# Kernel tuning notes

Measured on AMD Instinct MI355X. Metric: run time of the kernel, lower is better.

Reference implementation:

```python
import jax, jax.numpy as jnp
import numpy as np
from jax import lax
from jax.scipy.linalg import solve_triangular

T, DX, DZ = 8192, 1024, 16
POS_CONST = 1e-6
THRESH = 1e-5


def setup_inputs() -> dict:
    key = jax.random.key(0)
    ks = jax.random.split(key, 7)
    s = 0.02  # small init scale so A ~ I and AA is well-conditioned for Cholesky
    return {
        "X": jax.random.normal(ks[0], (T, DX), jnp.float32),
        "W1": jax.random.normal(ks[1], (DX, DX), jnp.float32) * s,
        "b1": jnp.zeros((DX,), jnp.float32),
        "Wmu": jax.random.normal(ks[2], (DX, DZ), jnp.float32) * s,
        "bmu": jnp.zeros((DZ,), jnp.float32),
        "WA": jax.random.normal(ks[3], (DX, DZ * DZ), jnp.float32) * s,
        "bA": jnp.zeros((DZ * DZ,), jnp.float32),
        "WB": jax.random.normal(ks[4], (2 * DX, DZ * DZ), jnp.float32) * s,
        "bB": jnp.zeros((DZ * DZ,), jnp.float32),
        "eps": jax.random.normal(ks[5], (T, DZ), jnp.float32),
    }


def _blk_tridag_chol(AA, BB):
    # AA: (T, d, d) diagonal blocks, BB: (T-1, d, d) lower off-diagonal blocks.
    # Returns lower-bidiagonal block Cholesky: chol_A (T,d,d), chol_B (T-1,d,d).
    L0 = jnp.linalg.cholesky(AA[0])

    def step(Lprev, ins):
        Bt, At = ins
        # C = Bt @ inv(Lprev)^T, via triangular solve: Lprev C^T = Bt^T
        C = solve_triangular(Lprev, Bt.T, lower=True).T
        Lt = jnp.linalg.cholesky(At - C @ C.T)
        return Lt, (Lt, C)

    _, (Ls, Cs) = lax.scan(step, L0, (BB, AA[1:]))
    return jnp.concatenate([L0[None], Ls]), Cs


def _blk_chol_inv_identity(chol_A, chol_B):
    # Forward substitution L x = b with b = block-diagonal identity blocks.
    I = jnp.eye(DZ, dtype=chol_A.dtype)
    x0 = solve_triangular(chol_A[0], I, lower=True)

    def step(xprev, ins):
        Lt, Ct = ins
        xt = solve_triangular(Lt, I - Ct @ xprev, lower=True)
        return xt, xt

    _, xs = lax.scan(step, x0, (chol_A[1:], chol_B))
    return jnp.concatenate([x0[None], xs])


def reference(X, W1, b1, Wmu, bmu, WA, bA, WB, bB, eps):
    # encode
    h = jax.nn.relu(X @ W1 + b1)                       # (T, dx)
    mu = h @ Wmu + bmu                                 # (T, dz)
    A = (h @ WA + bA).reshape(T, DZ, DZ) + jnp.eye(DZ, dtype=X.dtype)
    hcat = jnp.concatenate([h[1:], h[:-1]], axis=1)    # (T-1, 2*dx)
    B = (hcat @ WB + bB).reshape(T - 1, DZ, DZ)

    # make_psd
    diag_sq = jnp.einsum('tij,tkj->tik', A, A)         # A A^T
    offd_sq = jnp.einsum('tij,tkj->tik', B, B)         # B B^T
    offd_sq = jnp.concatenate([jnp.zeros((1, DZ, DZ), X.dtype), offd_sq])
    AA = diag_sq + offd_sq + POS_CONST * jnp.eye(DZ, dtype=X.dtype)
    BB = jnp.einsum('tij,tkj->tik', B, A[:-1])         # B A[:-1]^T

    chol_A, chol_B = _blk_tridag_chol(AA, BB)
    r = _blk_chol_inv_identity(chol_A, chol_B)         # (T, dz, dz)

    # relu(r - thresh) + thresh == max(r, thresh)
    r = jax.nn.relu(r - THRESH) + THRESH
    logdet = -jnp.log(jnp.einsum('tii->ti', r)).sum()
    entropy = logdet + DX * T / 2.0 * (1.0 + np.log(2.0 * np.pi))

    # sample_z = mu + r^T eps per block
    sample_z = mu + jnp.einsum('tji,tj->ti', r, eps)
    return entropy, sample_z
```

## Files before the change

### kernel.cpp

```cpp
#include <hip/hip_runtime.h>
#include <math.h>


#define T_STEPS 8192
#define DXX 1024

typedef __bf16 bf16x8 __attribute__((ext_vector_type(8)));
typedef float f32x4 __attribute__((ext_vector_type(4)));
typedef unsigned short u16x8 __attribute__((ext_vector_type(8)));
typedef unsigned short u16x4 __attribute__((ext_vector_type(4)));

#define DOT4(r, b) ((r).x*(b).x + (r).y*(b).y + (r).z*(b).z + (r).w*(b).w)

__device__ __forceinline__ unsigned short f2bf(float v) {
  unsigned int u = __float_as_uint(v);
  unsigned int r = (u + 0x7FFFu + ((u >> 16) & 1u)) >> 16;
  return (unsigned short)r;
}
__device__ __forceinline__ float bf2f(unsigned short b) {
  return __uint_as_float(((unsigned int)b) << 16);
}

__global__ __launch_bounds__(256) void to_bf16(
    const float* __restrict__ src, unsigned short* __restrict__ dst, int n4)
{
  int idx = blockIdx.x * 256 + threadIdx.x;
  if (idx >= n4) return;
  float4 v = ((const float4*)src)[idx];
  u16x4 h;
  h[0] = f2bf(v.x); h[1] = f2bf(v.y); h[2] = f2bf(v.z); h[3] = f2bf(v.w);
  *(u16x4*)(dst + (size_t)idx * 4) = h;
}

__global__ __launch_bounds__(256) void transpose_bf16(
    const float* __restrict__ W, unsigned short* __restrict__ Tt, int K, int N)
{
  __shared__ float tile[32][33];
  int k0 = blockIdx.x * 32, n0 = blockIdx.y * 32;
  int c = threadIdx.x & 31, r = threadIdx.x >> 5;
#pragma unroll
  for (int e = 0; e < 4; ++e)
    tile[r + 8 * e][c] = W[(size_t)(k0 + r + 8 * e) * N + n0 + c];
  __syncthreads();
#pragma unroll
  for (int e = 0; e < 4; ++e)
    Tt[(size_t)(n0 + r + 8 * e) * K + k0 + c] = f2bf(tile[c][r + 8 * e]);
}

#define LDT 40

__global__ __launch_bounds__(256) void gemm_mfma(
    const unsigned short* __restrict__ Abf, const unsigned short* __restrict__ Bbf,
    const float* __restrict__ bias, int biasN, float* __restrict__ outF,
    unsigned short* __restrict__ outBf, int M, int N, int K, int mode)
{
  __shared__ __align__(16) unsigned short At[128 * LDT];
  __shared__ __align__(16) unsigned short Bt[128 * LDT];
  int tid = threadIdx.x;
  int l = tid & 63;
  int w = tid >> 6;
  int wm = w >> 1, wn = w & 1;
  int lane15 = l & 15, quad = l >> 4;
  int bm = blockIdx.y * 128, bn = blockIdx.x * 128;
  int srow = tid >> 1, shalf = tid & 1;
  const size_t aRowOff = (size_t)(bm + srow) * K;
  const size_t bRowOff = (size_t)(bn + srow) * K;

  f32x4 acc[4][4];
#pragma unroll
  for (int mi = 0; mi < 4; ++mi)
#pragma unroll
    for (int ni = 0; ni < 4; ++ni) acc[mi][ni] = (f32x4){0.f, 0.f, 0.f, 0.f};

  for (int k0 = 0; k0 < K; k0 += 32) {
    u16x8 a0 = *(const u16x8*)(Abf + aRowOff + k0 + shalf * 16);
    u16x8 a1 = *(const u16x8*)(Abf + aRowOff + k0 + shalf * 16 + 8);
    u16x8 b0 = *(const u16x8*)(Bbf + bRowOff + k0 + shalf * 16);
    u16x8 b1 = *(const u16x8*)(Bbf + bRowOff + k0 + shalf * 16 + 8);
    __syncthreads();
    *(u16x8*)&At[srow * LDT + shalf * 16] = a0;
    *(u16x8*)&At[srow * LDT + shalf * 16 + 8] = a1;
    *(u16x8*)&Bt[srow * LDT + shalf * 16] = b0;
    *(u16x8*)&Bt[srow * LDT + shalf * 16 + 8] = b1;
    __syncthreads();
    bf16x8 af[4], bfr[4];
#pragma unroll
    for (int mi = 0; mi < 4; ++mi)
      af[mi] = *(const bf16x8*)&At[(wm * 64 + mi * 16 + lane15) * LDT + quad * 8];
#pragma unroll
    for (int ni = 0; ni < 4; ++ni)
      bfr[ni] = *(const bf16x8*)&Bt[(wn * 64 + ni * 16 + lane15) * LDT + quad * 8];
#pragma unroll
    for (int mi = 0; mi < 4; ++mi)
#pragma unroll
      for (int ni = 0; ni < 4; ++ni)
        acc[mi][ni] = __builtin_amdgcn_mfma_f32_16x16x32_bf16(af[mi], bfr[ni], acc[mi][ni], 0, 0, 0);
  }

#pragma unroll
  for (int mi = 0; mi < 4; ++mi) {
#pragma unroll
    for (int ni = 0; ni < 4; ++ni) {
      int gc = bn + wn * 64 + ni * 16 + lane15;
      float bv = (bias && gc < biasN) ? bias[gc] : 0.f;
#pragma unroll
      for (int r = 0; r < 4; ++r) {
        int gr = bm + wm * 64 + mi * 16 + quad * 4 + r;
        float v = acc[mi][ni][r] + bv;
        if (mode == 1) {
          outBf[(size_t)gr * N + gc] = f2bf(fmaxf(v, 0.f));
        } else {
          outF[(size_t)gr * N + gc] = v;
        }
      }
    }
  }
}

__global__ __launch_bounds__(256) void mu_gemm(
    const unsigned short* __restrict__ hbf, const float* __restrict__ Wmu,
    const float* __restrict__ bmu, float* __restrict__ mu)
{
  int idx = blockIdx.x * 256 + threadIdx.x;
  int t = idx >> 4, j = idx & 15;
  const u16x8* ph = (const u16x8*)(hbf + (size_t)t * 1024);
  float s = bmu[j];
#pragma unroll 2
  for (int k8 = 0; k8 < 128; ++k8) {
    u16x8 hv = ph[k8];
#pragma unroll
    for (int e = 0; e < 8; ++e)
      s = fmaf(bf2f(hv[e]), Wmu[(k8 * 8 + e) * 16 + j], s);
  }
  mu[idx] = s;
}

__global__ __launch_bounds__(256) void make_psd(
    const float* __restrict__ Ccat, const float* __restrict__ bB,
    float* __restrict__ AA, float* __restrict__ BBm, float* __restrict__ logdet)
{
  int t = blockIdx.x;
  int tid = threadIdx.x;
  int i = tid >> 4, j = tid & 15;
  if (t == 0 && tid == 0) *logdet = 0.f;
  __shared__ float a[16][17], bp[16][17], bq[16][17];
  a[i][j] = Ccat[(size_t)t * 768 + tid] + (i == j ? 1.f : 0.f);
  bp[i][j] = (t >= 1) ? (Ccat[(size_t)t * 768 + 256 + tid] + Ccat[(size_t)(t - 1) * 768 + 512 + tid] + bB[tid]) : 0.f;
  bool has_b = (t < T_STEPS - 1);
  if (has_b) bq[i][j] = Ccat[(size_t)(t + 1) * 768 + 256 + tid] + Ccat[(size_t)t * 768 + 512 + tid] + bB[tid];
  __syncthreads();
  float s = (i == j) ? 1e-6f : 0.f;
#pragma unroll
  for (int k = 0; k < 16; ++k) s += a[i][k] * a[j][k] + bp[i][k] * bp[j][k];
  AA[(size_t)t * 256 + tid] = s;
  if (has_b) {
    float s2 = 0.f;
#pragma unroll
    for (int k = 0; k < 16; ++k) s2 += bq[i][k] * a[j][k];
    BBm[(size_t)t * 256 + tid] = s2;
  }
}

#define RIC_S 4
#define RIC_W 16
#define RIC_NCH (T_STEPS / RIC_S)

__global__ __launch_bounds__(64) void riccati_wave(
    const float* __restrict__ AA, const float* __restrict__ BBm,
    float* __restrict__ D)
{
  int l = threadIdx.x;
  int q = l >> 4, c = l & 15;
  int p = blockIdx.x;
  int t0 = p * RIC_S;
  int tw = t0 - RIC_W; if (tw < 0) tw = 0;
  int tend = t0 + RIC_S - 1;
  int row = l >> 2, cb = (l & 3) * 4;

  __shared__ float bbs[320], dis[320], ys[320];

  float dr[4];
#pragma unroll
  for (int u = 0; u < 4; ++u)
    dr[u] = AA[(size_t)tw * 256 + (q * 4 + u) * 16 + c];

  for (int t = tw; ; ++t) {
    if (t >= t0) {
#pragma unroll
      for (int u = 0; u < 4; ++u)
        D[(size_t)t * 256 + (q * 4 + u) * 16 + c] = dr[u];
    }
    if (t == tend) break;
    float4 bb4 = *(const float4*)(BBm + (size_t)t * 256 + l * 4);
    float aar[4];
#pragma unroll
    for (int u = 0; u < 4; ++u)
      aar[u] = AA[(size_t)(t + 1) * 256 + (q * 4 + u) * 16 + c];

#pragma unroll
    for (int k = 0; k < 16; ++k) {
      const int kq = k >> 2, ku = k & 3;
      float rowv = __shfl(dr[ku], (kq << 4) | c);
      float pv   = __shfl(dr[ku], (kq << 4) | k);
      float cv0  = __shfl(dr[0], (l & 48) | k);
      float cv1  = __shfl(dr[1], (l & 48) | k);
      float cv2  = __shfl(dr[2], (l & 48) | k);
      float cv3  = __shfl(dr[3], (l & 48) | k);
      float rpv  = __builtin_amdgcn_rcpf(pv);
      float t1v  = rowv * rpv;
      float cva[4] = {cv0, cv1, cv2, cv3};
#pragma unroll
      for (int u = 0; u < 4; ++u) {
        bool irow = (q == kq) && (u == ku);
        float nv = irow ? ((c == k) ? rpv : t1v)
                        : ((c == k) ? (-cva[u] * rpv) : fmaf(-cva[u], t1v, dr[u]));
        dr[u] = nv;
      }
    }

    *(float4*)&bbs[row * 20 + cb] = bb4;
#pragma unroll
    for (int u = 0; u < 4; ++u) dis[(q * 4 + u) * 20 + c] = dr[u];

    float y0a = 0, y1a = 0, y2a = 0, y3a = 0;
    float y0b = 0, y1b = 0, y2b = 0, y3b = 0;
#pragma unroll
    for (int kb = 0; kb < 4; ++kb) {
      float4 bc4 = *(const float4*)&bbs[c * 20 + kb * 4];
      float4 r0 = *(const float4*)&dis[(q * 4 + 0) * 20 + kb * 4];
      float4 r1 = *(const float4*)&dis[(q * 4 + 1) * 20 + kb * 4];
      float4 r2 = *(const float4*)&dis[(q * 4 + 2) * 20 + kb * 4];
      float4 r3 = *(const float4*)&dis[(q * 4 + 3) * 20 + kb * 4];
      if (kb & 1) {
        y0b += DOT4(r0, bc4); y1b += DOT4(r1, bc4); y2b += DOT4(r2, bc4); y3b += DOT4(r3, bc4);
      } else {
        y0a += DOT4(r0, bc4); y1a += DOT4(r1, bc4); y2a += DOT4(r2, bc4); y3a += DOT4(r3, bc4);
      }
    }
    ys[(q * 4 + 0) * 20 + c] = y0a + y0b;
    ys[(q * 4 + 1) * 20 + c] = y1a + y1b;
    ys[(q * 4 + 2) * 20 + c] = y2a + y2b;
    ys[(q * 4 + 3) * 20 + c] = y3a + y3b;

    float s0a = aar[0], s1a = aar[1], s2a = aar[2], s3a = aar[3];
    float s0b = 0, s1b = 0, s2b = 0, s3b = 0;
#pragma unroll
    for (int kb = 0; kb < 4; ++kb) {
      float4 b0 = *(const float4*)&bbs[(q * 4 + 0) * 20 + kb * 4];
      float4 b1 = *(const float4*)&bbs[(q * 4 + 1) * 20 + kb * 4];
      float4 b2 = *(const float4*)&bbs[(q * 4 + 2) * 20 + kb * 4];
      float4 b3 = *(const float4*)&bbs[(q * 4 + 3) * 20 + kb * 4];
      float yk0 = ys[(kb * 4 + 0) * 20 + c];
      float yk1 = ys[(kb * 4 + 1) * 20 + c];
      float yk2 = ys[(kb * 4 + 2) * 20 + c];
      float yk3 = ys[(kb * 4 + 3) * 20 + c];
      if (kb & 1) {
        s0b -= b0.x * yk0 + b0.y * yk1 + b0.z * yk2 + b0.w * yk3;
        s1b -= b1.x * yk0 + b1.y * yk1 + b1.z * yk2 + b1.w * yk3;
        s2b -= b2.x * yk0 + b2.y * yk1 + b2.z * yk2 + b2.w * yk3;
        s3b -= b3.x * yk0 + b3.y * yk1 + b3.z * yk2 + b3.w * yk3;
      } else {
        s0a -= b0.x * yk0 + b0.y * yk1 + b0.z * yk2 + b0.w * yk3;
        s1a -= b1.x * yk0 + b1.y * yk1 + b1.z * yk2 + b1.w * yk3;
        s2a -= b2.x * yk0 + b2.y * yk1 + b2.z * yk2 + b2.w * yk3;
        s3a -= b3.x * yk0 + b3.y * yk1 + b3.z * yk2 + b3.w * yk3;
      }
    }
    dr[0] = s0a + s0b; dr[1] = s1a + s1b; dr[2] = s2a + s2b; dr[3] = s3a + s3b;
  }
}

__global__ __launch_bounds__(256) void chol_inv(
    const float* __restrict__ D, const float* __restrict__ BBm,
    float* __restrict__ Linv, float* __restrict__ Cmat)
{
  int t = blockIdx.x;
  int tid = threadIdx.x;
  int i = tid >> 4, j = tid & 15;
  __shared__ float d[16][17], li[16][17], rhs[16][17], bb[16][17];
  d[i][j] = D[(size_t)t * 256 + tid];
  bool has_b = (t < T_STEPS - 1);
  if (has_b) bb[i][j] = BBm[(size_t)t * 256 + tid];
  rhs[i][j] = (i == j) ? 1.f : 0.f;
  __syncthreads();
  for (int k = 0; k < 16; ++k) {
    if (tid == k * 16 + k) d[k][k] = sqrtf(d[k][k]);
    __syncthreads();
    if (j == k && i > k) d[i][k] /= d[k][k];
    __syncthreads();
    if (i > k && j > k && j <= i) d[i][j] -= d[i][k] * d[j][k];
    __syncthreads();
  }
  for (int k = 0; k < 16; ++k) {
    if (i == k) li[k][j] = rhs[k][j] / d[k][k];
    __syncthreads();
    if (i > k) rhs[i][j] -= d[i][k] * li[k][j];
    __syncthreads();
  }
  Linv[(size_t)t * 256 + tid] = li[i][j];
  if (has_b) {
    float s = 0.f;
#pragma unroll
    for (int k = 0; k < 16; ++k) s += bb[i][k] * li[j][k];
    Cmat[(size_t)t * 256 + tid] = s;
  }
}

__global__ __launch_bounds__(256) void gmat_kernel(
    const float* __restrict__ Linv, const float* __restrict__ Cmat,
    float* __restrict__ Gmat)
{
  int t = blockIdx.x;
  int tid = threadIdx.x;
  int i = tid >> 4, j = tid & 15;
  if (t == 0) { Gmat[tid] = 0.f; return; }
  __shared__ float li[16][17], cm[16][17];
  li[i][j] = Linv[(size_t)t * 256 + tid];
  cm[i][j] = Cmat[(size_t)(t - 1) * 256 + tid];
  __syncthreads();
  float s = 0.f;
#pragma unroll
  for (int k = 0; k < 16; ++k) s -= li[i][k] * cm[k][j];
  Gmat[(size_t)t * 256 + tid] = s;
}

#define XS 8
#define XW 32
#define XNCH (T_STEPS / XS)

__global__ __launch_bounds__(64) void xseq_g(
    const float* __restrict__ Linv, const float* __restrict__ Gmat,
    const float* __restrict__ mu, const float* __restrict__ eps,
    float* __restrict__ out, float* __restrict__ logdet)
{
  int l = threadIdx.x;
  int q = l >> 4, c = l & 15;
  int p = blockIdx.x;
  int t0 = p * XS;
  int ts = t0 - XW; if (ts < 0) ts = 0;
  int row = l >> 2, cb = (l & 3) * 4;
  __shared__ float gs[320];
  float xr[4] = {0.f, 0.f, 0.f, 0.f};
  float logacc = 0.f;

  float4 g4 = *(const float4*)(Gmat + (size_t)ts * 256 + l * 4);
  float li[4];
#pragma unroll
  for (int u = 0; u < 4; ++u)
    li[u] = Linv[(size_t)ts * 256 + (q * 4 + u) * 16 + c];

  for (int t = ts; t < t0 + XS; ++t) {
    float4 g4n = {0.f, 0.f, 0.f, 0.f};
    float lin[4] = {0.f, 0.f, 0.f, 0.f};
    if (t + 1 < t0 + XS) {
      g4n = *(const float4*)(Gmat + (size_t)(t + 1) * 256 + l * 4);
#pragma unroll
      for (int u = 0; u < 4; ++u)
        lin[u] = Linv[(size_t)(t + 1) * 256 + (q * 4 + u) * 16 + c];
    }
    *(float4*)&gs[row * 20 + cb] = g4;

    float x0a = li[0], x1a = li[1], x2a = li[2], x3a = li[3];
    float x0b = 0.f, x1b = 0.f, x2b = 0.f, x3b = 0.f;
#pragma unroll
    for (int kb = 0; kb < 4; ++kb) {
      float4 r0 = *(const float4*)&gs[(q * 4 + 0) * 20 + kb * 4];
      float4 r1 = *(const float4*)&gs[(q * 4 + 1) * 20 + kb * 4];
      float4 r2 = *(const float4*)&gs[(q * 4 + 2) * 20 + kb * 4];
      float4 r3 = *(const float4*)&gs[(q * 4 + 3) * 20 + kb * 4];
      float a0[4] = {r0.x, r0.y, r0.z, r0.w};
      float a1[4] = {r1.x, r1.y, r1.z, r1.w};
      float a2[4] = {r2.x, r2.y, r2.z, r2.w};
      float a3[4] = {r3.x, r3.y, r3.z, r3.w};
#pragma unroll
      for (int e = 0; e < 4; ++e) {
        float xk = __shfl(xr[e], (kb << 4) | c);
        if (kb & 1) {
          x0b = fmaf(a0[e], xk, x0b);
          x1b = fmaf(a1[e], xk, x1b);
          x2b = fmaf(a2[e], xk, x2b);
          x3b = fmaf(a3[e], xk, x3b);
        } else {
          x0a = fmaf(a0[e], xk, x0a);
          x1a = fmaf(a1[e], xk, x1a);
          x2a = fmaf(a2[e], xk, x2a);
          x3a = fmaf(a3[e], xk, x3a);
        }
      }
    }
    float x0 = x0a + x0b, x1 = x1a + x1b, x2 = x2a + x2b, x3 = x3a + x3b;
    xr[0] = x0; xr[1] = x1; xr[2] = x2; xr[3] = x3;

    if (t >= t0) {
      float r0v = fmaxf(x0, 1e-5f), r1v = fmaxf(x1, 1e-5f);
      float r2v = fmaxf(x2, 1e-5f), r3v = fmaxf(x3, 1e-5f);
      if (q == (c >> 2)) {
        int sel = c & 3;
        float dv = sel == 0 ? r0v : (sel == 1 ? r1v : (sel == 2 ? r2v : r3v));
        logacc -= logf(dv);
      }
      float e0 = eps[(size_t)t * 16 + q * 4 + 0];
      float e1 = eps[(size_t)t * 16 + q * 4 + 1];
      float e2 = eps[(size_t)t * 16 + q * 4 + 2];
      float e3 = eps[(size_t)t * 16 + q * 4 + 3];
      float part = r0v * e0 + r1v * e1 + r2v * e2 + r3v * e3;
      part += __shfl_xor(part, 16);
      part += __shfl_xor(part, 32);
      if (q == 0) out[1 + (size_t)t * 16 + c] = mu[(size_t)t * 16 + c] + part;
    }
    g4 = g4n;
    li[0] = lin[0]; li[1] = lin[1]; li[2] = lin[2]; li[3] = lin[3];
  }
#pragma unroll
  for (int off = 1; off < 64; off <<= 1) logacc += __shfl_xor(logacc, off);
  if (l == 0) atomicAdd(logdet, logacc);
}

__global__ void finalize_entropy(const float* __restrict__ logdet, float* __restrict__ out)
{
  if (threadIdx.x == 0 && blockIdx.x == 0) {
    const double ENT = 0.5 * 1024.0 * 8192.0 * (1.0 + 1.8378770664093454);
    out[0] = (float)(ENT + (double)(*logdet));
  }
}

extern "C" void kernel_launch(void* const* d_in, const int* in_sizes, int n_in,
                              void* d_out, int out_size, void* d_ws, size_t ws_size,
                              hipStream_t stream)
{
  const float* X   = (const float*)d_in[0];
  const float* W1  = (const float*)d_in[1];
  const float* b1  = (const float*)d_in[2];
  const float* Wmu = (const float*)d_in[3];
  const float* bmu = (const float*)d_in[4];
  const float* WA  = (const float*)d_in[5];
  const float* bA  = (const float*)d_in[6];
  const float* WB  = (const float*)d_in[7];
  const float* bB  = (const float*)d_in[8];
  const float* eps = (const float*)d_in[9];
  float* out = (float*)d_out;
  char* ws  = (char*)d_ws;

  unsigned short* Xbf  = (unsigned short*)(ws + 0);
  unsigned short* W1t  = (unsigned short*)(ws + 16777216);
  unsigned short* hbf  = (unsigned short*)(ws + 25165824);
  unsigned short* Wcat = (unsigned short*)(ws + 50856960);
  float* Ccat   = (float*)(ws + 0);
  float* Cmat   = (float*)(ws + 0);
  float* AAp    = (float*)(ws + 25165824);
  float* Linv   = (float*)(ws + 25165824);
  float* BBp    = (float*)(ws + 33554432);
  float* Dws    = (float*)(ws + 41943040);
  float* Gmat   = (float*)(ws + 41943040);
  float* muw    = (float*)(ws + 50331648);
  float* logdet = (float*)(ws + 50855936);

  dim3 blk(256);

  to_bf16<<<dim3(8192), blk, 0, stream>>>(X, Xbf, 8192 * 1024 / 4);
  transpose_bf16<<<dim3(32, 32), blk, 0, stream>>>(W1, W1t, 1024, 1024);
  transpose_bf16<<<dim3(32, 8), blk, 0, stream>>>(WA, Wcat, 1024, 256);
  transpose_bf16<<<dim3(32, 8), blk, 0, stream>>>(WB, Wcat + 256 * 1024, 1024, 256);
  transpose_bf16<<<dim3(32, 8), blk, 0, stream>>>(WB + 1024 * 256, Wcat + 512 * 1024, 1024, 256);
  gemm_mfma<<<dim3(8, 64), blk, 0, stream>>>(Xbf, W1t, b1, 1024, nullptr, hbf, 8192, 1024, 1024, 1);
  gemm_mfma<<<dim3(6, 64), blk, 0, stream>>>(hbf, Wcat, bA, 256, Ccat, nullptr, 8192, 768, 1024, 0);
  mu_gemm<<<dim3(512), blk, 0, stream>>>(hbf, Wmu, bmu, muw);
  make_psd<<<dim3(T_STEPS), blk, 0, stream>>>(Ccat, bB, AAp, BBp, logdet);
  riccati_wave<<<dim3(RIC_NCH), dim3(64), 0, stream>>>(AAp, BBp, Dws);
  chol_inv<<<dim3(T_STEPS), blk, 0, stream>>>(Dws, BBp, Linv, Cmat);
  gmat_kernel<<<dim3(T_STEPS), blk, 0, stream>>>(Linv, Cmat, Gmat);
  xseq_g<<<dim3(XNCH), dim3(64), 0, stream>>>(Linv, Gmat, muw, eps, out, logdet);
  finalize_entropy<<<dim3(1), dim3(64), 0, stream>>>(logdet, out);
}
```

Before: 380.9 us.

## Use direct global-to-LDS loads with swizzle in GEMM and retune Riccati kernel

```diff
diff --git a/kernel.cpp b/kernel.cpp
--- a/kernel.cpp
+++ b/kernel.cpp
@@ -10,6 +10,9 @@
 typedef unsigned short u16x8 __attribute__((ext_vector_type(8)));
 typedef unsigned short u16x4 __attribute__((ext_vector_type(4)));
 
+typedef __attribute__((address_space(1))) unsigned int as1_uint;
+typedef __attribute__((address_space(3))) unsigned int as3_uint;
+
 #define DOT4(r, b) ((r).x*(b).x + (r).y*(b).y + (r).z*(b).z + (r).w*(b).w)
 
 __device__ __forceinline__ unsigned short f2bf(float v) {
@@ -19,6 +22,10 @@
 }
 __device__ __forceinline__ float bf2f(unsigned short b) {
   return __uint_as_float(((unsigned int)b) << 16);
+}
+
+__device__ __forceinline__ void gload16(const unsigned short* g, unsigned short* s) {
+  __builtin_amdgcn_global_load_lds((as1_uint*)g, (as3_uint*)s, 16, 0, 0);
 }
 
 __global__ __launch_bounds__(256) void to_bf16(
@@ -47,24 +54,26 @@
     Tt[(size_t)(n0 + r + 8 * e) * K + k0 + c] = f2bf(tile[c][r + 8 * e]);
 }
 
-#define LDT 40
+#define GBK 64
 
 __global__ __launch_bounds__(256) void gemm_mfma(
     const unsigned short* __restrict__ Abf, const unsigned short* __restrict__ Bbf,
     const float* __restrict__ bias, int biasN, float* __restrict__ outF,
     unsigned short* __restrict__ outBf, int M, int N, int K, int mode)
 {
-  __shared__ __align__(16) unsigned short At[128 * LDT];
-  __shared__ __align__(16) unsigned short Bt[128 * LDT];
+  __shared__ __align__(16) unsigned short At[128 * GBK];
+  __shared__ __align__(16) unsigned short Bt[128 * GBK];
   int tid = threadIdx.x;
   int l = tid & 63;
   int w = tid >> 6;
   int wm = w >> 1, wn = w & 1;
   int lane15 = l & 15, quad = l >> 4;
   int bm = blockIdx.y * 128, bn = blockIdx.x * 128;
-  int srow = tid >> 1, shalf = tid & 1;
-  const size_t aRowOff = (size_t)(bm + srow) * K;
-  const size_t bRowOff = (size_t)(bn + srow) * K;
+
+  int srow = (w << 3) + (l >> 3);
+  int jswz = (l & 7) ^ (srow & 7);
+  const unsigned short* aSrc = Abf + (size_t)(bm + srow) * K + jswz * 8;
+  const unsigned short* bSrc = Bbf + (size_t)(bn + srow) * K + jswz * 8;
 
   f32x4 acc[4][4];
 #pragma unroll
@@ -72,29 +81,33 @@
 #pragma unroll
     for (int ni = 0; ni < 4; ++ni) acc[mi][ni] = (f32x4){0.f, 0.f, 0.f, 0.f};
 
-  for (int k0 = 0; k0 < K; k0 += 32) {
-    u16x8 a0 = *(const u16x8*)(Abf + aRowOff + k0 + shalf * 16);
-    u16x8 a1 = *(const u16x8*)(Abf + aRowOff + k0 + shalf * 16 + 8);
-    u16x8 b0 = *(const u16x8*)(Bbf + bRowOff + k0 + shalf * 16);
-    u16x8 b1 = *(const u16x8*)(Bbf + bRowOff + k0 + shalf * 16 + 8);
-    __syncthreads();
-    *(u16x8*)&At[srow * LDT + shalf * 16] = a0;
-    *(u16x8*)&At[srow * LDT + shalf * 16 + 8] = a1;
-    *(u16x8*)&Bt[srow * LDT + shalf * 16] = b0;
-    *(u16x8*)&Bt[srow * LDT + shalf * 16 + 8] = b1;
-    __syncthreads();
-    bf16x8 af[4], bfr[4];
-#pragma unroll
-    for (int mi = 0; mi < 4; ++mi)
-      af[mi] = *(const bf16x8*)&At[(wm * 64 + mi * 16 + lane15) * LDT + quad * 8];
-#pragma unroll
-    for (int ni = 0; ni < 4; ++ni)
-      bfr[ni] = *(const bf16x8*)&Bt[(wn * 64 + ni * 16 + lane15) * LDT + quad * 8];
-#pragma unroll
-    for (int mi = 0; mi < 4; ++mi)
-#pragma unroll
-      for (int ni = 0; ni < 4; ++ni)
-        acc[mi][ni] = __builtin_amdgcn_mfma_f32_16x16x32_bf16(af[mi], bfr[ni], acc[mi][ni], 0, 0, 0);
+  for (int k0 = 0; k0 < K; k0 += GBK) {
+#pragma unroll
+    for (int i = 0; i < 4; ++i) {
+      gload16(aSrc + (size_t)(i * 32) * K + k0, &At[(i * 32 + (w << 3)) * GBK]);
+      gload16(bSrc + (size_t)(i * 32) * K + k0, &Bt[(i * 32 + (w << 3)) * GBK]);
+    }
+    __syncthreads();
+#pragma unroll
+    for (int h = 0; h < 2; ++h) {
+      bf16x8 af[4], bfr[4];
+#pragma unroll
+      for (int mi = 0; mi < 4; ++mi) {
+        int r = wm * 64 + mi * 16 + lane15;
+        af[mi] = *(const bf16x8*)&At[r * GBK + ((((h << 2) + quad) ^ (lane15 & 7)) << 3)];
+      }
+#pragma unroll
+      for (int ni = 0; ni < 4; ++ni) {
+        int r = wn * 64 + ni * 16 + lane15;
+        bfr[ni] = *(const bf16x8*)&Bt[r * GBK + ((((h << 2) + quad) ^ (lane15 & 7)) << 3)];
+      }
+#pragma unroll
+      for (int mi = 0; mi < 4; ++mi)
+#pragma unroll
+        for (int ni = 0; ni < 4; ++ni)
+          acc[mi][ni] = __builtin_amdgcn_mfma_f32_16x16x32_bf16(af[mi], bfr[ni], acc[mi][ni], 0, 0, 0);
+    }
+    __syncthreads();
   }
 
 #pragma unroll
@@ -137,7 +150,7 @@
 
 __global__ __launch_bounds__(256) void make_psd(
     const float* __restrict__ Ccat, const float* __restrict__ bB,
-    float* __restrict__ AA, float* __restrict__ BBm, float* __restrict__ logdet)
+    float* __restrict__ AAT, float* __restrict__ BBm, float* __restrict__ logdet)
 {
   int t = blockIdx.x;
   int tid = threadIdx.x;
@@ -152,7 +165,7 @@
   float s = (i == j) ? 1e-6f : 0.f;
 #pragma unroll
   for (int k = 0; k < 16; ++k) s += a[i][k] * a[j][k] + bp[i][k] * bp[j][k];
-  AA[(size_t)t * 256 + tid] = s;
+  AAT[(size_t)t * 256 + ((i >> 2) * 64 + j * 4 + (i & 3))] = s;
   if (has_b) {
     float s2 = 0.f;
 #pragma unroll
@@ -161,12 +174,12 @@
   }
 }
 
-#define RIC_S 4
+#define RIC_S 8
 #define RIC_W 16
 #define RIC_NCH (T_STEPS / RIC_S)
 
 __global__ __launch_bounds__(64) void riccati_wave(
-    const float* __restrict__ AA, const float* __restrict__ BBm,
+    const float* __restrict__ AAT, const float* __restrict__ BBm,
     float* __restrict__ D)
 {
   int l = threadIdx.x;
@@ -179,10 +192,8 @@
 
   __shared__ float bbs[320], dis[320], ys[320];
 
-  float dr[4];
-#pragma unroll
-  for (int u = 0; u < 4; ++u)
-    dr[u] = AA[(size_t)tw * 256 + (q * 4 + u) * 16 + c];
+  float4 a4 = *(const float4*)(AAT + (size_t)tw * 256 + l * 4);
+  float dr[4] = {a4.x, a4.y, a4.z, a4.w};
 
   for (int t = tw; ; ++t) {
     if (t >= t0) {
@@ -192,16 +203,13 @@
     }
     if (t == tend) break;
     float4 bb4 = *(const float4*)(BBm + (size_t)t * 256 + l * 4);
-    float aar[4];
-#pragma unroll
-    for (int u = 0; u < 4; ++u)
-      aar[u] = AA[(size_t)(t + 1) * 256 + (q * 4 + u) * 16 + c];
+    float4 aar = *(const float4*)(AAT + (size_t)(t + 1) * 256 + l * 4);
 
 #pragma unroll
     for (int k = 0; k < 16; ++k) {
       const int kq = k >> 2, ku = k & 3;
       float rowv = __shfl(dr[ku], (kq << 4) | c);
-      float pv   = __shfl(dr[ku], (kq << 4) | k);
+      float pv   = __uint_as_float(__builtin_amdgcn_readlane(__float_as_uint(dr[ku]), (kq << 4) | k));
       float cv0  = __shfl(dr[0], (l & 48) | k);
       float cv1  = __shfl(dr[1], (l & 48) | k);
       float cv2  = __shfl(dr[2], (l & 48) | k);
@@ -242,7 +250,7 @@
     ys[(q * 4 + 2) * 20 + c] = y2a + y2b;
     ys[(q * 4 + 3) * 20 + c] = y3a + y3b;
 
-    float s0a = aar[0], s1a = aar[1], s2a = aar[2], s3a = aar[3];
+    float s0a = aar.x, s1a = aar.y, s2a = aar.z, s3a = aar.w;
     float s0b = 0, s1b = 0, s2b = 0, s3b = 0;
 #pragma unroll
     for (int kb = 0; kb < 4; ++kb) {
@@ -447,7 +455,7 @@
   unsigned short* Wcat = (unsigned short*)(ws + 50856960);
   float* Ccat   = (float*)(ws + 0);
   float* Cmat   = (float*)(ws + 0);
-  float* AAp    = (float*)(ws + 25165824);
+  float* AAT    = (float*)(ws + 25165824);
   float* Linv   = (float*)(ws + 25165824);
   float* BBp    = (float*)(ws + 33554432);
   float* Dws    = (float*)(ws + 41943040);
@@ -465,8 +473,8 @@
   gemm_mfma<<<dim3(8, 64), blk, 0, stream>>>(Xbf, W1t, b1, 1024, nullptr, hbf, 8192, 1024, 1024, 1);
   gemm_mfma<<<dim3(6, 64), blk, 0, stream>>>(hbf, Wcat, bA, 256, Ccat, nullptr, 8192, 768, 1024, 0);
   mu_gemm<<<dim3(512), blk, 0, stream>>>(hbf, Wmu, bmu, muw);
-  make_psd<<<dim3(T_STEPS), blk, 0, stream>>>(Ccat, bB, AAp, BBp, logdet);
-  riccati_wave<<<dim3(RIC_NCH), dim3(64), 0, stream>>>(AAp, BBp, Dws);
+  make_psd<<<dim3(T_STEPS), blk, 0, stream>>>(Ccat, bB, AAT, BBp, logdet);
+  riccati_wave<<<dim3(RIC_NCH), dim3(64), 0, stream>>>(AAT, BBp, Dws);
   chol_inv<<<dim3(T_STEPS), blk, 0, stream>>>(Dws, BBp, Linv, Cmat);
   gmat_kernel<<<dim3(T_STEPS), blk, 0, stream>>>(Linv, Cmat, Gmat);
   xseq_g<<<dim3(XNCH), dim3(64), 0, stream>>>(Linv, Gmat, muw, eps, out, logdet);
```

Result: faster. 364.7 us (-4.3%).
